# Kernel tuning notes

Measured on AMD Instinct MI355X. Metric: run time of the kernel, lower is better.

## Reference

```python
import jax, jax.numpy as jnp
import numpy as np

B, DM, L, N, K, EXP = 4, 256, 2048, 16, 4, 2
DIN = EXP * DM          # 512 = expand * d_model
DTR = (DM + 15) // 16   # 16, dt_rank = ceil(d_model/16)


def _conv_causal(x, w, b):
    # x: (B, DIN, L); depthwise causal conv, kernel K, left-pad K-1 (matches conv1d(padding=K-1)[..., :L])
    y = jax.lax.conv_general_dilated(x, w, (1,), [(w.shape[-1] - 1, 0)],
                                     dimension_numbers=('NCH', 'OIH', 'NCH'),
                                     feature_group_count=x.shape[1])
    return y + b[None, :, None]


def _ssm_branch(x, z, conv_w, conv_b, xproj_w, dt_w, dt_b, A_log, D):
    # One directional Mamba selective-scan branch. x, z: (B, DIN, L)
    u = jnp.swapaxes(jax.nn.silu(_conv_causal(x, conv_w, conv_b)), 1, 2)  # (B, L, DIN)
    x_dbl = u @ xproj_w.T                                                 # (B, L, DTR+2N)
    dt, Bm, Cm = jnp.split(x_dbl, [DTR, DTR + N], axis=-1)
    delta = jax.nn.softplus(dt @ dt_w.T + dt_b)                           # (B, L, DIN)
    A = -jnp.exp(A_log)                                                   # (DIN, N)
    dA = jnp.exp(delta[..., None] * A)                                    # (B, L, DIN, N)
    dBu = (delta * u)[..., None] * Bm[:, :, None, :]                      # (B, L, DIN, N)

    def step(h, inp):
        dA_t, dBu_t, C_t = inp
        h = dA_t * h + dBu_t                                              # (B, DIN, N)
        return h, jnp.einsum('bdn,bn->bd', h, C_t)

    h0 = jnp.zeros((u.shape[0], DIN, N), u.dtype)
    _, ys = jax.lax.scan(step, h0, (jnp.swapaxes(dA, 0, 1), jnp.swapaxes(dBu, 0, 1), jnp.swapaxes(Cm, 0, 1)))
    y = jnp.swapaxes(ys, 0, 1) + u * D                                    # (B, L, DIN)
    return y * jax.nn.silu(jnp.swapaxes(z, 1, 2))


def setup_inputs() -> dict:
    key = jax.random.key(0)
    ks = jax.random.split(key, 16)
    s = 0.02
    p = {}
    p['x'] = jax.random.normal(ks[0], (B, DM, 1, L), jnp.float32)
    p['in_proj_w'] = jax.random.normal(ks[1], (2 * DIN, DM), jnp.float32) * s
    A_init = jnp.log(jnp.broadcast_to(jnp.arange(1, N + 1, dtype=jnp.float32), (DIN, N)))
    for tag, i in (('', 2), ('_b', 9)):
        p['conv_w' + tag] = jax.random.normal(ks[i], (DIN, 1, K), jnp.float32) * s
        p['conv_b' + tag] = jnp.zeros((DIN,), jnp.float32)
        p['xproj_w' + tag] = jax.random.normal(ks[i + 1], (DTR + 2 * N, DIN), jnp.float32) * s
        p['dt_w' + tag] = jax.random.normal(ks[i + 2], (DIN, DTR), jnp.float32) * s
        p['dt_b' + tag] = jax.random.normal(ks[i + 3], (DIN,), jnp.float32) * s
        p['A_log' + tag] = A_init
        p['D' + tag] = jnp.ones((DIN,), jnp.float32)
    p['out_proj_w'] = jax.random.normal(ks[8], (DM, DIN), jnp.float32) * s
    return p


def reference(x, in_proj_w, conv_w, conv_b, xproj_w, dt_w, dt_b, A_log, D,
              conv_w_b, conv_b_b, xproj_w_b, dt_w_b, dt_b_b, A_log_b, D_b, out_proj_w):
    x_res = x
    h = jnp.swapaxes(jnp.squeeze(x, 2), 1, 2)        # (B, L, DM)
    xz = jnp.swapaxes(h @ in_proj_w.T, 1, 2)         # (B, 2*DIN, L)
    xf, z = xz[:, :DIN], xz[:, DIN:]
    y_f = _ssm_branch(xf, z, conv_w, conv_b, xproj_w, dt_w, dt_b, A_log, D)
    y_b = _ssm_branch(jnp.flip(xf, -1), jnp.flip(z, -1),
                      conv_w_b, conv_b_b, xproj_w_b, dt_w_b, dt_b_b, A_log_b, D_b)
    y = y_f + jnp.flip(y_b, 1)                       # (B, L, DIN) : bimamba v2 fuse
    out = y @ out_proj_w.T                           # (B, L, DM)
    out = jnp.swapaxes(out, 1, 2).reshape(-1, DM, 1, L)
    return out + x_res
```

## Files before the change

kernel.cpp:

```cpp
#include <hip/hip_runtime.h>
#include <math.h>

#define B_    4
#define DM_   256
#define L_    2048
#define NS_   16
#define DIN_  512
#define LC_   16
#define NC_   128
#define BLD_  ((size_t)B_ * L_ * DIN_)

typedef __bf16 bf16x8 __attribute__((ext_vector_type(8)));
typedef float f32x4 __attribute__((ext_vector_type(4)));

__device__ __forceinline__ float silu_f(float x) { return x / (1.0f + __expf(-x)); }
__device__ __forceinline__ float softplus_f(float x) {
    return fmaxf(x, 0.0f) + __logf(1.0f + __expf(-fabsf(x)));
}
__device__ __forceinline__ unsigned short f2bf(float f) {
    unsigned int u = __float_as_uint(f);
    unsigned int r = (u + 0x7fffu + ((u >> 16) & 1u)) >> 16;
    return (unsigned short)r;
}
__device__ __forceinline__ float bf2f(unsigned short h) {
    return __uint_as_float(((unsigned int)h) << 16);
}
__device__ __forceinline__ void unpack8(uint4 p, float* v) {
    v[0] = bf2f((unsigned short)(p.x & 0xffff)); v[1] = bf2f((unsigned short)(p.x >> 16));
    v[2] = bf2f((unsigned short)(p.y & 0xffff)); v[3] = bf2f((unsigned short)(p.y >> 16));
    v[4] = bf2f((unsigned short)(p.z & 0xffff)); v[5] = bf2f((unsigned short)(p.z >> 16));
    v[6] = bf2f((unsigned short)(p.w & 0xffff)); v[7] = bf2f((unsigned short)(p.w >> 16));
}
__device__ __forceinline__ void unpack8_s(uint4 p, float* v) {
    const unsigned sx = __builtin_amdgcn_readfirstlane(p.x);
    const unsigned sy = __builtin_amdgcn_readfirstlane(p.y);
    const unsigned sz = __builtin_amdgcn_readfirstlane(p.z);
    const unsigned sw = __builtin_amdgcn_readfirstlane(p.w);
    v[0] = __uint_as_float(sx << 16); v[1] = __uint_as_float(sx & 0xffff0000u);
    v[2] = __uint_as_float(sy << 16); v[3] = __uint_as_float(sy & 0xffff0000u);
    v[4] = __uint_as_float(sz << 16); v[5] = __uint_as_float(sz & 0xffff0000u);
    v[6] = __uint_as_float(sw << 16); v[7] = __uint_as_float(sw & 0xffff0000u);
}
__device__ __forceinline__ uint4 pack8(const float* v) {
    uint4 p;
    p.x = (unsigned)f2bf(v[0]) | ((unsigned)f2bf(v[1]) << 16);
    p.y = (unsigned)f2bf(v[2]) | ((unsigned)f2bf(v[3]) << 16);
    p.z = (unsigned)f2bf(v[4]) | ((unsigned)f2bf(v[5]) << 16);
    p.w = (unsigned)f2bf(v[6]) | ((unsigned)f2bf(v[7]) << 16);
    return p;
}
__device__ __forceinline__ void pow16(float r, float* e) {
    e[0] = r;
    e[1] = r * r;
    e[3] = e[1] * e[1];
    e[7] = e[3] * e[3];
    e[15] = e[7] * e[7];
    e[2] = e[1] * e[0];
    e[4] = e[3] * e[0];
    e[5] = e[3] * e[1];
    e[6] = e[3] * e[2];
    e[8] = e[7] * e[0];
    e[9] = e[7] * e[1];
    e[10] = e[7] * e[2];
    e[11] = e[7] * e[3];
    e[12] = e[7] * e[4];
    e[13] = e[7] * e[5];
    e[14] = e[7] * e[6];
}

#define GLL(gp, lp) __builtin_amdgcn_global_load_lds( \
    (const __attribute__((address_space(1))) void*)(gp), \
    (__attribute__((address_space(3))) void*)(lp), 16, 0, 0)

__global__ __launch_bounds__(256) void k_prep(
    const float* __restrict__ x, const float* __restrict__ Win,
    const float* __restrict__ Wo,
    const float* __restrict__ xpw0, const float* __restrict__ xpw1,
    unsigned short* __restrict__ A16, unsigned short* __restrict__ W16,
    unsigned short* __restrict__ Wo2, unsigned short* __restrict__ W2)
{
    __shared__ float t[64][65];
    const int bid = blockIdx.x;
    const int tid = threadIdx.x;
    if (bid < 512) {
        const int kb = bid & 3;
        const int lb = (bid >> 2) & 31;
        const int b  = bid >> 7;
        const int k0 = kb * 64, l0 = lb * 64;
        const int ll = tid & 63;
        const int kg = tid >> 6;
#pragma unroll
        for (int r = 0; r < 16; ++r) {
            const int kl = kg * 16 + r;
            t[kl][ll] = x[((size_t)b * DM_ + k0 + kl) * L_ + l0 + ll];
        }
        __syncthreads();
        const int k2 = (tid & 31) * 2;
        const int lg = tid >> 5;
#pragma unroll
        for (int r = 0; r < 8; ++r) {
            const int l2 = lg + r * 8;
            unsigned p = (unsigned)f2bf(t[k2][l2]) | ((unsigned)f2bf(t[k2 + 1][l2]) << 16);
            *(unsigned*)&A16[((size_t)b * L_ + l0 + l2) * DM_ + k0 + k2] = p;
        }
        return;
    }
    if (bid < 640) {
        const int g = (bid - 512) * 256 + tid;
        const float4 v0 = ((const float4*)Win)[g * 2];
        const float4 v1 = ((const float4*)Win)[g * 2 + 1];
        float v[8] = {v0.x, v0.y, v0.z, v0.w, v1.x, v1.y, v1.z, v1.w};
        ((uint4*)W16)[g] = pack8(v);
        return;
    }
    if (bid < 768) {
        const int g = (bid - 640) * 256 + tid;
        const int n  = g >> 7;
        const int k0 = (g & 127) * 8;
        const int ks = k0 & 511;
        const float4 v0 = *(const float4*)&Wo[(size_t)n * 512 + ks];
        const float4 v1 = *(const float4*)&Wo[(size_t)n * 512 + ks + 4];
        float v[8] = {v0.x, v0.y, v0.z, v0.w, v1.x, v1.y, v1.z, v1.w};
        *(uint4*)&Wo2[(size_t)n * 1024 + k0] = pack8(v);
        return;
    }
    {
        const int g = (bid - 768) * 256 + tid;
        const int br  = g >> 12;
        const int rem = g & 4095;
        const int d   = rem >> 6;
        const int k0  = (rem & 63) * 8;
        const float* xpw = br ? xpw1 : xpw0;
        float v[8];
        if (d < 48) {
#pragma unroll
            for (int j = 0; j < 8; ++j) v[j] = xpw[(size_t)d * 512 + k0 + j];
        } else {
#pragma unroll
            for (int j = 0; j < 8; ++j) v[j] = 0.0f;
        }
        *(uint4*)&W2[((size_t)br * 64 + d) * 512 + k0] = pack8(v);
    }
}

__global__ __launch_bounds__(256) void k_mm_in(
    const unsigned short* __restrict__ A16, const unsigned short* __restrict__ W16,
    unsigned short* __restrict__ xf16, unsigned short* __restrict__ zs16)
{
    __shared__ __align__(16) short As[128 * 32];
    __shared__ __align__(16) short Bs[128 * 32];
    const int tid = threadIdx.x;
    const int mb = blockIdx.x & 63;
    const int nb = blockIdx.x >> 6;
    const int m0 = mb * 128, n0 = nb * 128;
    const int w = tid >> 6, lane = tid & 63;
    const int wm = w & 1, wn = w >> 1;
    const int l16 = lane & 15, kq = lane >> 4;
    const int arow = lane >> 2;
    const int ac8 = (lane & 3) * 8;

    f32x4 acc[4][4];
#pragma unroll
    for (int i = 0; i < 4; ++i)
#pragma unroll
        for (int j = 0; j < 4; ++j) acc[i][j] = (f32x4){0.f, 0.f, 0.f, 0.f};

    for (int k0 = 0; k0 < 256; k0 += 32) {
#pragma unroll
        for (int r = 0; r < 2; ++r) {
            const int rb = r * 64 + w * 16;
            GLL(&A16[(size_t)(m0 + rb + arow) * 256 + k0 + ac8], &As[rb * 32]);
            GLL(&W16[(size_t)(n0 + rb + arow) * 256 + k0 + ac8], &Bs[rb * 32]);
        }
        __syncthreads();
        bf16x8 a[4], bq[4];
#pragma unroll
        for (int f = 0; f < 4; ++f) {
            a[f]  = *(const bf16x8*)&As[(wm * 64 + f * 16 + l16) * 32 + kq * 8];
            bq[f] = *(const bf16x8*)&Bs[(wn * 64 + f * 16 + l16) * 32 + kq * 8];
        }
#pragma unroll
        for (int i = 0; i < 4; ++i)
#pragma unroll
            for (int j = 0; j < 4; ++j)
                acc[i][j] = __builtin_amdgcn_mfma_f32_16x16x32_bf16(a[i], bq[j], acc[i][j], 0, 0, 0);
        __syncthreads();
    }

    const bool isX = (n0 < DIN_);
#pragma unroll
    for (int i = 0; i < 4; ++i) {
        const int row = m0 + wm * 64 + i * 16 + kq * 4;
#pragma unroll
        for (int j = 0; j < 4; ++j) {
            const int col = n0 + wn * 64 + j * 16 + l16;
#pragma unroll
            for (int q = 0; q < 4; ++q) {
                const float v = acc[i][j][q];
                if (isX) xf16[(size_t)(row + q) * DIN_ + col] = f2bf(v);
                else     zs16[(size_t)(row + q) * DIN_ + col - DIN_] = f2bf(silu_f(v));
            }
        }
    }
}

__global__ __launch_bounds__(256) void k_conv(
    const unsigned short* __restrict__ xf16,
    const float* __restrict__ cw0, const float* __restrict__ cw1,
    const float* __restrict__ cb0, const float* __restrict__ cb1,
    unsigned short* __restrict__ u16b)
{
    const int br = blockIdx.y;
    const float* cw = br ? cw1 : cw0;
    const float* cb = br ? cb1 : cb0;
    unsigned short* u16 = u16b + (size_t)br * BLD_;

    const int g  = blockIdx.x * 256 + threadIdx.x;
    const int d8 = g & 63;
    const int tl = g >> 6;
    const int t  = tl & (L_ - 1);
    const int b  = tl >> 11;
    const int d0 = d8 * 8;

    float wr[8][4];
#pragma unroll
    for (int dd = 0; dd < 8; ++dd) {
        const float4 w = *(const float4*)&cw[(size_t)(d0 + dd) * 4];
        wr[dd][0] = w.x; wr[dd][1] = w.y; wr[dd][2] = w.z; wr[dd][3] = w.w;
    }
    float acc[8];
    {
        const float4 b0 = *(const float4*)&cb[d0];
        const float4 b1 = *(const float4*)&cb[d0 + 4];
        acc[0] = b0.x; acc[1] = b0.y; acc[2] = b0.z; acc[3] = b0.w;
        acc[4] = b1.x; acc[5] = b1.y; acc[6] = b1.z; acc[7] = b1.w;
    }
#pragma unroll
    for (int k = 0; k < 4; ++k) {
        const int idx = br ? (L_ - 1 - t) + 3 - k : t - 3 + k;
        if (idx >= 0 && idx < L_) {
            const uint4 xp = *(const uint4*)&xf16[((size_t)b * L_ + idx) * DIN_ + d0];
            float xv[8];
            unpack8(xp, xv);
#pragma unroll
            for (int dd = 0; dd < 8; ++dd) acc[dd] += xv[dd] * wr[dd][k];
        }
    }
    float o[8];
#pragma unroll
    for (int dd = 0; dd < 8; ++dd) o[dd] = silu_f(acc[dd]);
    *(uint4*)&u16[(size_t)tl * DIN_ + d0] = pack8(o);
}

__global__ __launch_bounds__(256) void k_mm_x(
    const unsigned short* __restrict__ u16b, const unsigned short* __restrict__ W2base,
    unsigned short* __restrict__ dtr16b, unsigned short* __restrict__ bc16b)
{
    const int br = blockIdx.y;
    const unsigned short* u16 = u16b + (size_t)br * BLD_;
    const unsigned short* W2  = W2base + (size_t)br * 64 * DIN_;
    unsigned short* dtr16 = dtr16b + (size_t)br * B_ * L_ * 16;
    unsigned short* bc16  = bc16b  + (size_t)br * B_ * L_ * 32;

    __shared__ __align__(16) short As[32 * 64];
    __shared__ __align__(16) short Bs[64 * 64];
    const int tid = threadIdx.x;
    const int m0 = blockIdx.x * 32;
    const int w = tid >> 6, lane = tid & 63;
    const int wm = w & 1, wn = w >> 1;
    const int l16 = lane & 15, kq = lane >> 4;
    const int lr8 = lane >> 3;
    const int sw8 = ((lane & 7) ^ (lr8 & 7)) * 8;

    f32x4 acc[2];
    acc[0] = (f32x4){0.f, 0.f, 0.f, 0.f};
    acc[1] = (f32x4){0.f, 0.f, 0.f, 0.f};

    for (int k0 = 0; k0 < 512; k0 += 64) {
        GLL(&u16[(size_t)(m0 + w * 8 + lr8) * 512 + k0 + sw8], &As[w * 8 * 64]);
        GLL(&W2[(size_t)(w * 16 + lr8) * 512 + k0 + sw8],      &Bs[(w * 16) * 64]);
        GLL(&W2[(size_t)(w * 16 + 8 + lr8) * 512 + k0 + sw8],  &Bs[(w * 16 + 8) * 64]);
        __syncthreads();
        bf16x8 a[2], bq[2][2];
#pragma unroll
        for (int ks = 0; ks < 2; ++ks) {
            const int sa = ((ks * 4 + kq) ^ (l16 & 7)) * 8;
            a[ks]     = *(const bf16x8*)&As[(wm * 16 + l16) * 64 + sa];
            bq[0][ks] = *(const bf16x8*)&Bs[(wn * 32 + l16) * 64 + sa];
            bq[1][ks] = *(const bf16x8*)&Bs[(wn * 32 + 16 + l16) * 64 + sa];
        }
#pragma unroll
        for (int j = 0; j < 2; ++j)
#pragma unroll
            for (int ks = 0; ks < 2; ++ks)
                acc[j] = __builtin_amdgcn_mfma_f32_16x16x32_bf16(a[ks], bq[j][ks], acc[j], 0, 0, 0);
        __syncthreads();
    }

#pragma unroll
    for (int j = 0; j < 2; ++j) {
        const int col = wn * 32 + j * 16 + l16;
        const int row = m0 + wm * 16 + kq * 4;
#pragma unroll
        for (int q = 0; q < 4; ++q) {
            const float v = acc[j][q];
            if (col < 16)       dtr16[(size_t)(row + q) * 16 + col] = f2bf(v);
            else if (col < 48)  bc16[(size_t)(row + q) * 32 + (col - 16)] = f2bf(v);
        }
    }
}

__global__ __launch_bounds__(256) void k_mm_out(
    const unsigned short* __restrict__ Wo2, const unsigned short* __restrict__ ypair,
    const float* __restrict__ xres, float* __restrict__ out)
{
    __shared__ __align__(16) short As[64 * 64];
    __shared__ __align__(16) short Bs[64 * 64];
    const int tid = threadIdx.x;
    const int mb = blockIdx.x & 127;
    const int nb = blockIdx.x >> 7;
    const int m0 = mb * 64, n0 = nb * 64;
    const int w = tid >> 6, lane = tid & 63;
    const int wm = w & 1, wn = w >> 1;
    const int l16 = lane & 15, kq = lane >> 4;
    const int lr8 = lane >> 3;
    const int sw8 = ((lane & 7) ^ (lr8 & 7)) * 8;

    f32x4 acc[2][2];
#pragma unroll
    for (int i = 0; i < 2; ++i)
#pragma unroll
        for (int j = 0; j < 2; ++j) acc[i][j] = (f32x4){0.f, 0.f, 0.f, 0.f};

    for (int k0 = 0; k0 < 1024; k0 += 64) {
        GLL(&Wo2[(size_t)(n0 + w * 16 + lr8) * 1024 + k0 + sw8],      &As[(w * 16) * 64]);
        GLL(&Wo2[(size_t)(n0 + w * 16 + 8 + lr8) * 1024 + k0 + sw8],  &As[(w * 16 + 8) * 64]);
        GLL(&ypair[(size_t)(m0 + w * 16 + lr8) * 1024 + k0 + sw8],     &Bs[(w * 16) * 64]);
        GLL(&ypair[(size_t)(m0 + w * 16 + 8 + lr8) * 1024 + k0 + sw8], &Bs[(w * 16 + 8) * 64]);
        __syncthreads();
        bf16x8 a[2][2], bq[2][2];
#pragma unroll
        for (int ks = 0; ks < 2; ++ks) {
            const int sa = ((ks * 4 + kq) ^ (l16 & 7)) * 8;
            a[0][ks]  = *(const bf16x8*)&As[(wm * 32 + l16) * 64 + sa];
            a[1][ks]  = *(const bf16x8*)&As[(wm * 32 + 16 + l16) * 64 + sa];
            bq[0][ks] = *(const bf16x8*)&Bs[(wn * 32 + l16) * 64 + sa];
            bq[1][ks] = *(const bf16x8*)&Bs[(wn * 32 + 16 + l16) * 64 + sa];
        }
#pragma unroll
        for (int i = 0; i < 2; ++i)
#pragma unroll
            for (int j = 0; j < 2; ++j)
#pragma unroll
                for (int ks = 0; ks < 2; ++ks)
                    acc[i][j] = __builtin_amdgcn_mfma_f32_16x16x32_bf16(a[i][ks], bq[j][ks], acc[i][j], 0, 0, 0);
        __syncthreads();
    }

    const int b = m0 >> 11;
    const int l0 = m0 & (L_ - 1);
#pragma unroll
    for (int i = 0; i < 2; ++i) {
        const int n = n0 + wm * 32 + i * 16 + kq * 4;
#pragma unroll
        for (int j = 0; j < 2; ++j) {
            const int l = l0 + wn * 32 + j * 16 + l16;
#pragma unroll
            for (int q = 0; q < 4; ++q) {
                const size_t o = ((size_t)b * DM_ + n + q) * L_ + l;
                out[o] = acc[i][j][q] + xres[o];
            }
        }
    }
}

__global__ __launch_bounds__(256) void k_scan1(
    const unsigned short* __restrict__ dtr16b, const unsigned short* __restrict__ u16b,
    const unsigned short* __restrict__ bc16b,
    const float* __restrict__ dtw0, const float* __restrict__ dtw1,
    const float* __restrict__ dtb0, const float* __restrict__ dtb1,
    float* __restrict__ Rcb, unsigned short* __restrict__ S16b,
    unsigned short* __restrict__ de16b)
{
    const int bi    = blockIdx.x;
    const int half  = bi & 1;
    const int chunk = (bi >> 1) & (NC_ - 1);
    const int b     = (bi >> 8) & 3;
    const int br    = bi >> 10;
    const int d     = half * 256 + threadIdx.x;

    const unsigned short* dtr16 = dtr16b + (size_t)br * B_ * L_ * 16;
    const unsigned short* u16   = u16b + (size_t)br * BLD_;
    const unsigned short* bc16  = bc16b + (size_t)br * B_ * L_ * 32;
    const float* dtw = br ? dtw1 : dtw0;
    const float bb   = (br ? dtb1 : dtb0)[d];
    float* Rc           = Rcb + (size_t)br * B_ * NC_ * DIN_;
    unsigned short* S16 = S16b + (size_t)br * B_ * NC_ * DIN_ * 16;
    unsigned short* de16 = de16b + (size_t)br * BLD_;

    float dtwd[16];
#pragma unroll
    for (int q = 0; q < 4; ++q) {
        const float4 v = *(const float4*)&dtw[(size_t)d * 16 + q * 4];
        dtwd[4*q] = v.x; dtwd[4*q+1] = v.y; dtwd[4*q+2] = v.z; dtwd[4*q+3] = v.w;
    }

    float Rp = 1.0f, Sr[16];
#pragma unroll
    for (int n = 0; n < 16; ++n) Sr[n] = 0.0f;

    const size_t tl0 = (size_t)b * L_ + chunk * LC_;
    size_t td = tl0 * DIN_ + d;
    size_t tg = tl0 * 32;
    size_t tr = tl0 * 16;
#pragma unroll
    for (int tt = 0; tt < LC_; ++tt, td += DIN_, tg += 32, tr += 16) {
        const float uu = bf2f(u16[td]);
        float dr[16];
        unpack8_s(*(const uint4*)&dtr16[tr],     dr);
        unpack8_s(*(const uint4*)&dtr16[tr + 8], dr + 8);
        float pre = bb;
#pragma unroll
        for (int rr = 0; rr < 16; ++rr) pre = fmaf(dr[rr], dtwd[rr], pre);
        const float de = softplus_f(pre);
        const float du = de * uu;
        float bm[16];
        unpack8_s(*(const uint4*)&bc16[tg],     bm);
        unpack8_s(*(const uint4*)&bc16[tg + 8], bm + 8);
        const float r = exp2f(-de * 1.4426950408889634f);
        de16[td] = f2bf(de);
        float e[16];
        pow16(r, e);
        Rp *= r;
#pragma unroll
        for (int n = 0; n < 16; ++n)
            Sr[n] = Sr[n] * e[n] + du * bm[n];
    }
    const size_t oc = ((size_t)b * NC_ + chunk) * DIN_ + d;
    Rc[oc] = Rp;
    *(uint4*)&S16[oc * 16]     = pack8(Sr);
    *(uint4*)&S16[oc * 16 + 8] = pack8(Sr + 8);
}

#define PF_ 4
__global__ __launch_bounds__(256) void k_prefix(
    const float* __restrict__ Rcb, const unsigned short* __restrict__ S16b,
    unsigned short* __restrict__ Hin16b)
{
    const int g  = blockIdx.x * 256 + threadIdx.x;
    const int n  = g & 15;
    const int d  = (g >> 4) & (DIN_ - 1);
    const int b  = (g >> 13) & 3;
    const int br = (g >> 15) & 1;
    const int m  = n + 1;

    const float* Rc = Rcb + (size_t)br * B_ * NC_ * DIN_;
    const unsigned short* S16 = S16b + (size_t)br * B_ * NC_ * DIN_ * 16;
    unsigned short* Hin16     = Hin16b + (size_t)br * B_ * NC_ * DIN_ * 16;

    size_t oc = (size_t)b * NC_ * DIN_ + d;
    float rc[PF_], s[PF_];
#pragma unroll
    for (int i = 0; i < PF_; ++i) {
        rc[i] = Rc[oc + (size_t)i * DIN_];
        s[i]  = bf2f(S16[(oc + (size_t)i * DIN_) * 16 + n]);
    }
    float h = 0.0f;
    for (int c = 0; c < NC_; c += PF_) {
        float rcn[PF_], sn[PF_];
        if (c + PF_ < NC_) {
#pragma unroll
            for (int i = 0; i < PF_; ++i) {
                rcn[i] = Rc[oc + (size_t)(PF_ + i) * DIN_];
                sn[i]  = bf2f(S16[(oc + (size_t)(PF_ + i) * DIN_) * 16 + n]);
            }
        }
#pragma unroll
        for (int i = 0; i < PF_; ++i) {
            const float r1 = rc[i];
            float p  = (m & 1) ? r1 : 1.0f;
            float b1 = r1 * r1; if (m & 2)  p *= b1;
            float b2 = b1 * b1; if (m & 4)  p *= b2;
            float b3 = b2 * b2; if (m & 8)  p *= b3;
            float b4 = b3 * b3; if (m & 16) p *= b4;
            Hin16[(oc + (size_t)i * DIN_) * 16 + n] = f2bf(h);
            h = p * h + s[i];
        }
        oc += (size_t)PF_ * DIN_;
#pragma unroll
        for (int i = 0; i < PF_; ++i) { rc[i] = rcn[i]; s[i] = sn[i]; }
    }
}

__global__ __launch_bounds__(256) void k_scan2(
    const unsigned short* __restrict__ u16b, const unsigned short* __restrict__ bc16b,
    const unsigned short* __restrict__ de16b,
    const float* __restrict__ Dp0, const float* __restrict__ Dp1,
    const unsigned short* __restrict__ Hin16b, const unsigned short* __restrict__ zs16,
    unsigned short* __restrict__ ypair)
{
    const int bi    = blockIdx.x;
    const int half  = bi & 1;
    const int chunk = (bi >> 1) & (NC_ - 1);
    const int b     = (bi >> 8) & 3;
    const int br    = bi >> 10;
    const int d     = half * 256 + threadIdx.x;

    const unsigned short* u16   = u16b + (size_t)br * BLD_;
    const unsigned short* bc16  = bc16b + (size_t)br * B_ * L_ * 32;
    const unsigned short* de16  = de16b + (size_t)br * BLD_;
    const unsigned short* Hin16 = Hin16b + (size_t)br * B_ * NC_ * DIN_ * 16;
    const float Dv = (br ? Dp1 : Dp0)[d];

    float h[16];
    const size_t oc = ((size_t)b * NC_ + chunk) * DIN_ + d;
    unpack8(*(const uint4*)&Hin16[oc * 16],     h);
    unpack8(*(const uint4*)&Hin16[oc * 16 + 8], h + 8);

    const size_t tl0 = (size_t)b * L_ + chunk * LC_;
    size_t td = tl0 * DIN_ + d;
    size_t tg = tl0 * 32;
#pragma unroll 8
    for (int tt = 0; tt < LC_; ++tt, td += DIN_, tg += 32) {
        const int t = chunk * LC_ + tt;
        const float uu = bf2f(u16[td]);
        const float de = bf2f(de16[td]);
        const float r  = exp2f(-de * 1.4426950408889634f);
        const float du = de * uu;
        float bm[16], cm[16];
        unpack8_s(*(const uint4*)&bc16[tg],      bm);
        unpack8_s(*(const uint4*)&bc16[tg + 8],  bm + 8);
        unpack8_s(*(const uint4*)&bc16[tg + 16], cm);
        unpack8_s(*(const uint4*)&bc16[tg + 24], cm + 8);
        float e[16];
        pow16(r, e);
        float yac = 0.0f;
#pragma unroll
        for (int n = 0; n < 16; ++n) {
            h[n] = h[n] * e[n] + du * bm[n];
            yac += h[n] * cm[n];
        }
        const int pos = br ? (L_ - 1 - t) : t;
        const size_t oz = ((size_t)b * L_ + pos) * DIN_ + d;
        const size_t oy = ((size_t)b * L_ + pos) * 1024 + br * 512 + d;
        ypair[oy] = f2bf((yac + uu * Dv) * bf2f(zs16[oz]));
    }
}

extern "C" void kernel_launch(void* const* d_in, const int* in_sizes, int n_in,
                              void* d_out, int out_size, void* d_ws, size_t ws_size,
                              hipStream_t stream)
{
    (void)in_sizes; (void)n_in; (void)out_size; (void)ws_size;
    const float* x      = (const float*)d_in[0];
    const float* Win    = (const float*)d_in[1];
    const float* cw[2]  = {(const float*)d_in[2],  (const float*)d_in[9]};
    const float* cb[2]  = {(const float*)d_in[3],  (const float*)d_in[10]};
    const float* xpw[2] = {(const float*)d_in[4],  (const float*)d_in[11]};
    const float* dtw[2] = {(const float*)d_in[5],  (const float*)d_in[12]};
    const float* dtb[2] = {(const float*)d_in[6],  (const float*)d_in[13]};
    const float* Dp[2]  = {(const float*)d_in[8],  (const float*)d_in[15]};
    const float* Wo     = (const float*)d_in[16];
    float* out = (float*)d_out;

    unsigned short* us = (unsigned short*)d_ws;
    unsigned short* xf16  = us;  us += BLD_;
    unsigned short* zs16  = us;  us += BLD_;
    unsigned short* u16   = us;  us += 2 * BLD_;
    unsigned short* ypair = us;  us += 2 * BLD_;
    unsigned short* de16  = us;  us += 2 * BLD_;
    unsigned short* dtr16 = us;  us += (size_t)2 * B_ * L_ * 16;
    unsigned short* bc16  = us;  us += (size_t)2 * B_ * L_ * 32;
    unsigned short* S16   = us;  us += (size_t)2 * B_ * NC_ * DIN_ * 16;
    unsigned short* Hin16 = us;  us += (size_t)2 * B_ * NC_ * DIN_ * 16;
    unsigned short* A16   = us;  us += (size_t)B_ * L_ * DM_;
    unsigned short* W16   = us;  us += (size_t)2 * DIN_ * DM_;
    unsigned short* Wo2   = us;  us += (size_t)DM_ * 1024;
    unsigned short* W2    = us;  us += (size_t)2 * 64 * DIN_;
    float* Rc = (float*)us;

    k_prep<<<800, 256, 0, stream>>>(x, Win, Wo, xpw[0], xpw[1], A16, W16, Wo2, W2);
    k_mm_in<<<512, 256, 0, stream>>>(A16, W16, xf16, zs16);
    k_conv<<<dim3(B_ * L_ * 64 / 256, 2), 256, 0, stream>>>(xf16, cw[0], cw[1], cb[0], cb[1], u16);
    k_mm_x<<<dim3(256, 2), 256, 0, stream>>>(u16, W2, dtr16, bc16);
    k_scan1<<<B_ * NC_ * 4, 256, 0, stream>>>(dtr16, u16, bc16, dtw[0], dtw[1],
                                              dtb[0], dtb[1], Rc, S16, de16);
    k_prefix<<<(B_ * DIN_ * NS_ * 2) / 256, 256, 0, stream>>>(Rc, S16, Hin16);
    k_scan2<<<B_ * NC_ * 4, 256, 0, stream>>>(u16, bc16, de16, Dp[0], Dp[1],
                                              Hin16, zs16, ypair);
    k_mm_out<<<512, 256, 0, stream>>>(Wo2, ypair, x, out);
}
```

Before: 157.2 us.

## Fuse causal conv into x-projection GEMM and stage B/C/dt rows in LDS

Merges the depthwise conv+SiLU kernel into the x_proj GEMM kernel. The conv output tile is written straight into a full-K shared-memory A buffer (32x512) as well as to global, so the GEMM no longer reloads u from global, and one launch goes away. The scan kernels now load the per-chunk dt-rank and B/C rows into LDS once per block instead of each thread reading them from global. They also get launch_bounds with 8 blocks per CU. Trade-offs: the fused kernel launches only 512 blocks and uses 40KB of LDS, and the occupancy hint can force register pressure or spills in the scan kernels.

```diff
diff --git a/kernel.cpp b/kernel.cpp
--- a/kernel.cpp
+++ b/kernel.cpp
@@ -204,68 +204,73 @@
     }
 }
 
-__global__ __launch_bounds__(256) void k_conv(
+__global__ __launch_bounds__(256) void k_cmx(
     const unsigned short* __restrict__ xf16,
     const float* __restrict__ cw0, const float* __restrict__ cw1,
     const float* __restrict__ cb0, const float* __restrict__ cb1,
-    unsigned short* __restrict__ u16b)
+    const unsigned short* __restrict__ W2base,
+    unsigned short* __restrict__ u16b,
+    unsigned short* __restrict__ dtr16b, unsigned short* __restrict__ bc16b)
 {
     const int br = blockIdx.y;
     const float* cw = br ? cw1 : cw0;
     const float* cb = br ? cb1 : cb0;
-    unsigned short* u16 = u16b + (size_t)br * BLD_;
-
-    const int g  = blockIdx.x * 256 + threadIdx.x;
-    const int d8 = g & 63;
-    const int tl = g >> 6;
-    const int t  = tl & (L_ - 1);
-    const int b  = tl >> 11;
-    const int d0 = d8 * 8;
-
-    float wr[8][4];
-#pragma unroll
-    for (int dd = 0; dd < 8; ++dd) {
-        const float4 w = *(const float4*)&cw[(size_t)(d0 + dd) * 4];
-        wr[dd][0] = w.x; wr[dd][1] = w.y; wr[dd][2] = w.z; wr[dd][3] = w.w;
-    }
-    float acc[8];
-    {
-        const float4 b0 = *(const float4*)&cb[d0];
-        const float4 b1 = *(const float4*)&cb[d0 + 4];
-        acc[0] = b0.x; acc[1] = b0.y; acc[2] = b0.z; acc[3] = b0.w;
-        acc[4] = b1.x; acc[5] = b1.y; acc[6] = b1.z; acc[7] = b1.w;
-    }
-#pragma unroll
-    for (int k = 0; k < 4; ++k) {
-        const int idx = br ? (L_ - 1 - t) + 3 - k : t - 3 + k;
-        if (idx >= 0 && idx < L_) {
-            const uint4 xp = *(const uint4*)&xf16[((size_t)b * L_ + idx) * DIN_ + d0];
-            float xv[8];
-            unpack8(xp, xv);
-#pragma unroll
-            for (int dd = 0; dd < 8; ++dd) acc[dd] += xv[dd] * wr[dd][k];
-        }
-    }
-    float o[8];
-#pragma unroll
-    for (int dd = 0; dd < 8; ++dd) o[dd] = silu_f(acc[dd]);
-    *(uint4*)&u16[(size_t)tl * DIN_ + d0] = pack8(o);
-}
-
-__global__ __launch_bounds__(256) void k_mm_x(
-    const unsigned short* __restrict__ u16b, const unsigned short* __restrict__ W2base,
-    unsigned short* __restrict__ dtr16b, unsigned short* __restrict__ bc16b)
-{
-    const int br = blockIdx.y;
-    const unsigned short* u16 = u16b + (size_t)br * BLD_;
-    const unsigned short* W2  = W2base + (size_t)br * 64 * DIN_;
+    const unsigned short* W2 = W2base + (size_t)br * 64 * DIN_;
+    unsigned short* u16   = u16b + (size_t)br * BLD_;
     unsigned short* dtr16 = dtr16b + (size_t)br * B_ * L_ * 16;
     unsigned short* bc16  = bc16b  + (size_t)br * B_ * L_ * 32;
 
-    __shared__ __align__(16) short As[32 * 64];
+    __shared__ __align__(16) short As[32 * 512];
     __shared__ __align__(16) short Bs[64 * 64];
+
     const int tid = threadIdx.x;
     const int m0 = blockIdx.x * 32;
+
+    {
+        const int r  = tid >> 3;
+        const int g0 = tid & 7;
+        const int t  = (m0 + r) & (L_ - 1);
+        const int b  = (m0 + r) >> 11;
+        int idxs[4];
+#pragma unroll
+        for (int k = 0; k < 4; ++k)
+            idxs[k] = br ? (L_ - 1 - t) + 3 - k : t - 3 + k;
+#pragma unroll
+        for (int rep = 0; rep < 8; ++rep) {
+            const int d0 = g0 * 8 + rep * 64;
+            float acc[8];
+            {
+                const float4 b0 = *(const float4*)&cb[d0];
+                const float4 b1 = *(const float4*)&cb[d0 + 4];
+                acc[0]=b0.x; acc[1]=b0.y; acc[2]=b0.z; acc[3]=b0.w;
+                acc[4]=b1.x; acc[5]=b1.y; acc[6]=b1.z; acc[7]=b1.w;
+            }
+            float wr[8][4];
+#pragma unroll
+            for (int dd = 0; dd < 8; ++dd) {
+                const float4 w = *(const float4*)&cw[(size_t)(d0 + dd) * 4];
+                wr[dd][0]=w.x; wr[dd][1]=w.y; wr[dd][2]=w.z; wr[dd][3]=w.w;
+            }
+#pragma unroll
+            for (int k = 0; k < 4; ++k) {
+                const int idx = idxs[k];
+                if (idx >= 0 && idx < L_) {
+                    const uint4 xp = *(const uint4*)&xf16[((size_t)b * L_ + idx) * DIN_ + d0];
+                    float xv[8]; unpack8(xp, xv);
+#pragma unroll
+                    for (int dd = 0; dd < 8; ++dd) acc[dd] += xv[dd] * wr[dd][k];
+                }
+            }
+            float o[8];
+#pragma unroll
+            for (int dd = 0; dd < 8; ++dd) o[dd] = silu_f(acc[dd]);
+            const uint4 p = pack8(o);
+            *(uint4*)&u16[(size_t)(m0 + r) * DIN_ + d0] = p;
+            *(uint4*)&As[r * 512 + (d0 ^ ((r & 7) * 8))] = p;
+        }
+    }
+    __syncthreads();
+
     const int w = tid >> 6, lane = tid & 63;
     const int wm = w & 1, wn = w >> 1;
     const int l16 = lane & 15, kq = lane >> 4;
@@ -277,15 +282,14 @@
     acc[1] = (f32x4){0.f, 0.f, 0.f, 0.f};
 
     for (int k0 = 0; k0 < 512; k0 += 64) {
-        GLL(&u16[(size_t)(m0 + w * 8 + lr8) * 512 + k0 + sw8], &As[w * 8 * 64]);
-        GLL(&W2[(size_t)(w * 16 + lr8) * 512 + k0 + sw8],      &Bs[(w * 16) * 64]);
-        GLL(&W2[(size_t)(w * 16 + 8 + lr8) * 512 + k0 + sw8],  &Bs[(w * 16 + 8) * 64]);
+        GLL(&W2[(size_t)(w * 16 + lr8) * 512 + k0 + sw8],     &Bs[(w * 16) * 64]);
+        GLL(&W2[(size_t)(w * 16 + 8 + lr8) * 512 + k0 + sw8], &Bs[(w * 16 + 8) * 64]);
         __syncthreads();
         bf16x8 a[2], bq[2][2];
 #pragma unroll
         for (int ks = 0; ks < 2; ++ks) {
             const int sa = ((ks * 4 + kq) ^ (l16 & 7)) * 8;
-            a[ks]     = *(const bf16x8*)&As[(wm * 16 + l16) * 64 + sa];
+            a[ks]     = *(const bf16x8*)&As[(wm * 16 + l16) * 512 + k0 + sa];
             bq[0][ks] = *(const bf16x8*)&Bs[(wn * 32 + l16) * 64 + sa];
             bq[1][ks] = *(const bf16x8*)&Bs[(wn * 32 + 16 + l16) * 64 + sa];
         }
@@ -374,7 +378,7 @@
     }
 }
 
-__global__ __launch_bounds__(256) void k_scan1(
+__global__ __launch_bounds__(256, 8) void k_scan1(
     const unsigned short* __restrict__ dtr16b, const unsigned short* __restrict__ u16b,
     const unsigned short* __restrict__ bc16b,
     const float* __restrict__ dtw0, const float* __restrict__ dtw1,
@@ -394,9 +398,18 @@
     const unsigned short* bc16  = bc16b + (size_t)br * B_ * L_ * 32;
     const float* dtw = br ? dtw1 : dtw0;
     const float bb   = (br ? dtb1 : dtb0)[d];
-    float* Rc           = Rcb + (size_t)br * B_ * NC_ * DIN_;
-    unsigned short* S16 = S16b + (size_t)br * B_ * NC_ * DIN_ * 16;
+    float* Rc            = Rcb + (size_t)br * B_ * NC_ * DIN_;
+    unsigned short* S16  = S16b + (size_t)br * B_ * NC_ * DIN_ * 16;
     unsigned short* de16 = de16b + (size_t)br * BLD_;
+
+    __shared__ __align__(16) unsigned short sdtr[LC_ * 16];
+    __shared__ __align__(16) unsigned short sbc[LC_ * 32];
+    const size_t tl0 = (size_t)b * L_ + chunk * LC_;
+    if (threadIdx.x < 32)
+        ((uint4*)sdtr)[threadIdx.x] = *(const uint4*)&dtr16[tl0 * 16 + threadIdx.x * 8];
+    else if (threadIdx.x < 96)
+        ((uint4*)sbc)[threadIdx.x - 32] = *(const uint4*)&bc16[tl0 * 32 + (threadIdx.x - 32) * 8];
+    __syncthreads();
 
     float dtwd[16];
 #pragma unroll
@@ -409,24 +422,21 @@
 #pragma unroll
     for (int n = 0; n < 16; ++n) Sr[n] = 0.0f;
 
-    const size_t tl0 = (size_t)b * L_ + chunk * LC_;
     size_t td = tl0 * DIN_ + d;
-    size_t tg = tl0 * 32;
-    size_t tr = tl0 * 16;
-#pragma unroll
-    for (int tt = 0; tt < LC_; ++tt, td += DIN_, tg += 32, tr += 16) {
+#pragma unroll
+    for (int tt = 0; tt < LC_; ++tt, td += DIN_) {
         const float uu = bf2f(u16[td]);
         float dr[16];
-        unpack8_s(*(const uint4*)&dtr16[tr],     dr);
-        unpack8_s(*(const uint4*)&dtr16[tr + 8], dr + 8);
+        unpack8_s(*(const uint4*)&sdtr[tt * 16],     dr);
+        unpack8_s(*(const uint4*)&sdtr[tt * 16 + 8], dr + 8);
         float pre = bb;
 #pragma unroll
         for (int rr = 0; rr < 16; ++rr) pre = fmaf(dr[rr], dtwd[rr], pre);
         const float de = softplus_f(pre);
         const float du = de * uu;
         float bm[16];
-        unpack8_s(*(const uint4*)&bc16[tg],     bm);
-        unpack8_s(*(const uint4*)&bc16[tg + 8], bm + 8);
+        unpack8_s(*(const uint4*)&sbc[tt * 32],     bm);
+        unpack8_s(*(const uint4*)&sbc[tt * 32 + 8], bm + 8);
         const float r = exp2f(-de * 1.4426950408889634f);
         de16[td] = f2bf(de);
         float e[16];
@@ -492,7 +502,7 @@
     }
 }
 
-__global__ __launch_bounds__(256) void k_scan2(
+__global__ __launch_bounds__(256, 8) void k_scan2(
     const unsigned short* __restrict__ u16b, const unsigned short* __restrict__ bc16b,
     const unsigned short* __restrict__ de16b,
     const float* __restrict__ Dp0, const float* __restrict__ Dp1,
@@ -512,26 +522,30 @@
     const unsigned short* Hin16 = Hin16b + (size_t)br * B_ * NC_ * DIN_ * 16;
     const float Dv = (br ? Dp1 : Dp0)[d];
 
+    __shared__ __align__(16) unsigned short sbc[LC_ * 32];
+    const size_t tl0 = (size_t)b * L_ + chunk * LC_;
+    if (threadIdx.x < 64)
+        ((uint4*)sbc)[threadIdx.x] = *(const uint4*)&bc16[tl0 * 32 + threadIdx.x * 8];
+    __syncthreads();
+
     float h[16];
     const size_t oc = ((size_t)b * NC_ + chunk) * DIN_ + d;
     unpack8(*(const uint4*)&Hin16[oc * 16],     h);
     unpack8(*(const uint4*)&Hin16[oc * 16 + 8], h + 8);
 
-    const size_t tl0 = (size_t)b * L_ + chunk * LC_;
     size_t td = tl0 * DIN_ + d;
-    size_t tg = tl0 * 32;
-#pragma unroll 8
-    for (int tt = 0; tt < LC_; ++tt, td += DIN_, tg += 32) {
+#pragma unroll
+    for (int tt = 0; tt < LC_; ++tt, td += DIN_) {
         const int t = chunk * LC_ + tt;
         const float uu = bf2f(u16[td]);
         const float de = bf2f(de16[td]);
         const float r  = exp2f(-de * 1.4426950408889634f);
         const float du = de * uu;
         float bm[16], cm[16];
-        unpack8_s(*(const uint4*)&bc16[tg],      bm);
-        unpack8_s(*(const uint4*)&bc16[tg + 8],  bm + 8);
-        unpack8_s(*(const uint4*)&bc16[tg + 16], cm);
-        unpack8_s(*(const uint4*)&bc16[tg + 24], cm + 8);
+        unpack8_s(*(const uint4*)&sbc[tt * 32],      bm);
+        unpack8_s(*(const uint4*)&sbc[tt * 32 + 8],  bm + 8);
+        unpack8_s(*(const uint4*)&sbc[tt * 32 + 16], cm);
+        unpack8_s(*(const uint4*)&sbc[tt * 32 + 24], cm + 8);
         float e[16];
         pow16(r, e);
         float yac = 0.0f;
@@ -581,8 +595,8 @@
 
     k_prep<<<800, 256, 0, stream>>>(x, Win, Wo, xpw[0], xpw[1], A16, W16, Wo2, W2);
     k_mm_in<<<512, 256, 0, stream>>>(A16, W16, xf16, zs16);
-    k_conv<<<dim3(B_ * L_ * 64 / 256, 2), 256, 0, stream>>>(xf16, cw[0], cw[1], cb[0], cb[1], u16);
-    k_mm_x<<<dim3(256, 2), 256, 0, stream>>>(u16, W2, dtr16, bc16);
+    k_cmx<<<dim3(256, 2), 256, 0, stream>>>(xf16, cw[0], cw[1], cb[0], cb[1],
+                                            W2, u16, dtr16, bc16);
     k_scan1<<<B_ * NC_ * 4, 256, 0, stream>>>(dtr16, u16, bc16, dtw[0], dtw[1],
                                               dtb[0], dtb[1], Rc, S16, de16);
     k_prefix<<<(B_ * DIN_ * NS_ * 2) / 256, 256, 0, stream>>>(Rc, S16, Hin16);
```

Result: slower. 244.7 us (+55.7%).
